# Kernel optimization log

Hardware: AMD Instinct MI355X
Metric: run time of the kernel (lower is better)

The kernel has to match this reference:

```python
import jax, jax.numpy as jnp
import numpy as np

B, T, D, H = 256, 256, 512, 8
HD = D // H  # 64


def _rope_tables(t, hd):
    pos = jnp.arange(t, dtype=jnp.float32)
    inv_freq = 1.0 / (10000.0 ** (jnp.arange(0, hd, 2, dtype=jnp.float32) / hd))
    ang = pos[:, None] * inv_freq[None, :]            # (T, hd/2)
    cos = jnp.repeat(jnp.cos(ang), 2, axis=-1)        # (T, hd) interleaved pairs
    sin = jnp.repeat(jnp.sin(ang), 2, axis=-1)
    return cos, sin


def setup_inputs() -> dict:
    key = jax.random.key(0)
    k1, k2, k3 = jax.random.split(key, 3)
    x = jax.random.normal(k1, (B, T, D), dtype=jnp.float32)
    cos, sin = _rope_tables(T, HD)
    Wqkv = jax.random.normal(k2, (3 * D, D), dtype=jnp.float32) * 0.02
    Wout = jax.random.normal(k3, (D, D), dtype=jnp.float32) * 0.02
    return {"x": x, "cos": cos, "sin": sin, "Wqkv": Wqkv, "Wout": Wout}


def _apply_rope(x, cos, sin):
    # x: (B, T, H, hd); cos/sin: (T, hd)
    x1 = x[..., 0::2]
    x2 = x[..., 1::2]
    rot = jnp.stack((-x2, x1), axis=-1).reshape(x.shape)  # interleaved rotate
    return x * cos[None, :, None, :] + rot * sin[None, :, None, :]


def reference(x, cos, sin, Wqkv, Wout):
    b, t, d = x.shape
    qkv = (x @ Wqkv.T).reshape(b, t, 3, H, HD)
    q, k, v = qkv[:, :, 0], qkv[:, :, 1], qkv[:, :, 2]   # (B, T, H, hd)
    q = _apply_rope(q, cos[:t], sin[:t])
    k = _apply_rope(k, cos[:t], sin[:t])
    q = q.transpose(0, 2, 1, 3)  # (B, H, T, hd)
    k = k.transpose(0, 2, 1, 3)
    v = v.transpose(0, 2, 1, 3)
    scale = 1.0 / jnp.sqrt(jnp.float32(HD))
    scores = jnp.einsum('bhqd,bhkd->bhqk', q, k) * scale
    causal = jnp.arange(t)[:, None] >= jnp.arange(t)[None, :]  # (T, T)
    scores = jnp.where(causal[None, None], scores, jnp.finfo(scores.dtype).min)
    att = jax.nn.softmax(scores, axis=-1)
    out = jnp.einsum('bhqk,bhkd->bhqd', att, v)          # (B, H, T, hd)
    out = out.transpose(0, 2, 1, 3).reshape(b, t, d)
    return out @ Wout.T
```

## Files before the change

kernel.cpp:

```cpp
#include <hip/hip_runtime.h>

typedef float floatx4 __attribute__((ext_vector_type(4)));
typedef short short8 __attribute__((ext_vector_type(8)));
typedef unsigned short ushort_t;

#define AS1 __attribute__((address_space(1)))
#define AS3 __attribute__((address_space(3)))

__device__ __forceinline__ void gload_lds16(const ushort_t* g, ushort_t* l) {
    __builtin_amdgcn_global_load_lds((const AS1 unsigned int*)g, (AS3 unsigned int*)l, 16, 0, 0);
}

__device__ __forceinline__ ushort_t f2bf(float f) {
    union { float f; unsigned u; } v; v.f = f;
    unsigned r = v.u + 0x7FFFu + ((v.u >> 16) & 1u);
    return (ushort_t)(r >> 16);
}

#define KDIM 512
#define LOG2E 1.44269504f

#define XB_OFF   0ull
#define ATT_OFF  0ull
#define WQKV_OFF 33554432ull
#define WOUT_OFF 34340864ull
#define QB_OFF   34603008ull
#define KB_OFF   68157440ull
#define VB_OFF   101711872ull

__global__ __launch_bounds__(256) void convert_k(
    const float* __restrict__ x, const float* __restrict__ wqkv,
    const float* __restrict__ wout, ushort_t* __restrict__ dst)
{
    size_t i = (size_t)blockIdx.x * 256 + threadIdx.x;
    size_t e = i * 4;
    const float* s; size_t o;
    if (e < 33554432ull)      { s = x;    o = e; }
    else if (e < 34340864ull) { s = wqkv; o = e - 33554432ull; }
    else                      { s = wout; o = e - 34340864ull; }
    float4 v = *(const float4*)(s + o);
    ushort4 r;
    r.x = f2bf(v.x); r.y = f2bf(v.y); r.z = f2bf(v.z); r.w = f2bf(v.w);
    *(ushort4*)(dst + e) = r;
}

template <int EPI>
__global__ __launch_bounds__(256, 3) void gemm_bt(
    const ushort_t* __restrict__ A, const ushort_t* __restrict__ Bw,
    float* __restrict__ Cf,
    ushort_t* __restrict__ qout, ushort_t* __restrict__ kout, ushort_t* __restrict__ vout,
    const float* __restrict__ cosT, const float* __restrict__ sinT)
{
    __shared__ __align__(16) ushort_t As[128 * 64];
    __shared__ __align__(16) ushort_t Bs[128 * 64];
    const int bn = blockIdx.x, bm = blockIdx.y;
    const int tid = threadIdx.x;
    const int lane = tid & 63, wave = tid >> 6;
    const int wm = wave & 1, wn = wave >> 1;
    const int quad = lane >> 4, l16 = lane & 15;

    const ushort_t* Ag = A + (size_t)bm * 128 * KDIM;
    const ushort_t* Bg = Bw + (size_t)bn * 128 * KDIM;

    floatx4 acc[4][4] = {};

    for (int k0 = 0; k0 < KDIM; k0 += 64) {
#pragma unroll
        for (int ii = 0; ii < 4; ii++) {
            int e8 = ii * 256 + tid;
            int row = e8 >> 3, col = (e8 & 7) << 3;
            gload_lds16(Ag + row * KDIM + k0 + col, &As[e8 * 8]);
            gload_lds16(Bg + row * KDIM + k0 + col, &Bs[e8 * 8]);
        }
        __syncthreads();
#pragma unroll
        for (int kk = 0; kk < 2; kk++) {
            short8 af[4], bf[4];
#pragma unroll
            for (int mi = 0; mi < 4; mi++)
                af[mi] = *(const short8*)&As[(wm * 64 + mi * 16 + l16) * 64 + kk * 32 + quad * 8];
#pragma unroll
            for (int ni = 0; ni < 4; ni++)
                bf[ni] = *(const short8*)&Bs[(wn * 64 + ni * 16 + l16) * 64 + kk * 32 + quad * 8];
#pragma unroll
            for (int mi = 0; mi < 4; mi++)
#pragma unroll
                for (int ni = 0; ni < 4; ni++)
                    acc[mi][ni] = __builtin_amdgcn_mfma_f32_16x16x32_bf16(
                        af[mi], bf[ni], acc[mi][ni], 0, 0, 0);
        }
        __syncthreads();
    }

    if constexpr (EPI == 1) {
        const int n_base = bn * 128 + wn * 64;
        const int qkv = n_base >> 9;
        ushort_t* dst = (qkv == 0) ? qout : (qkv == 1 ? kout : vout);
#pragma unroll
        for (int mi = 0; mi < 4; mi++) {
            const int m = bm * 128 + wm * 64 + mi * 16 + quad * 4;
#pragma unroll
            for (int ni = 0; ni < 4; ni++) {
                const int n = n_base + ni * 16 + l16;
                const int nw = n & 511, hd = n & 63;
#pragma unroll
                for (int r = 0; r < 4; r++) {
                    const int mm = m + r, t = mm & 255;
                    const size_t dsti = (size_t)mm * 512 + nw;
                    float val = acc[mi][ni][r];
                    if (qkv == 2) {
                        dst[dsti] = f2bf(val);
                    } else {
                        float partner = __shfl_xor(val, 1);
                        float c = cosT[t * 64 + hd], s = sinT[t * 64 + hd];
                        float o = val * c + ((hd & 1) ? partner : -partner) * s;
                        dst[dsti] = (qkv == 0) ? f2bf(o * 0.125f) : f2bf(o);
                    }
                }
            }
        }
    } else {
#pragma unroll
        for (int mi = 0; mi < 4; mi++) {
            const int m = bm * 128 + wm * 64 + mi * 16 + quad * 4;
#pragma unroll
            for (int ni = 0; ni < 4; ni++) {
                const int n = bn * 128 + wn * 64 + ni * 16 + l16;
#pragma unroll
                for (int r = 0; r < 4; r++)
                    Cf[(size_t)(m + r) * 512 + n] = acc[mi][ni][r];
            }
        }
    }
}

__global__ __launch_bounds__(256) void attn_k(
    const ushort_t* __restrict__ qb, const ushort_t* __restrict__ kb,
    const ushort_t* __restrict__ vb, ushort_t* __restrict__ attb)
{
    __shared__ __align__(16) ushort_t Ks[256 * 72];
    __shared__ __align__(16) ushort_t Vt[64 * 264];
    __shared__ __align__(16) ushort_t Ps[4 * 32 * 40];

    const int blk = blockIdx.x;
    const int qt = blk & 1, bh = blk >> 1;
    const int b = bh >> 3, h = bh & 7;
    const int tid = threadIdx.x, lane = tid & 63, w = tid >> 6;
    const int quad = lane >> 4, l16 = lane & 15;
    const int q0 = qt * 128;
    const int kend = q0 + 128;

    const ushort_t* Kg = kb + ((size_t)b * 256) * 512 + h * 64;
    const ushort_t* Vg = vb + ((size_t)b * 256) * 512 + h * 64;
    const ushort_t* Qg = qb + ((size_t)b * 256) * 512 + h * 64;

    for (int e8 = tid; e8 < kend * 8; e8 += 256) {
        int t = e8 >> 3, c = (e8 & 7) << 3;
        *(short8*)&Ks[t * 72 + c] = *(const short8*)&Kg[t * 512 + c];
        short8 vv = *(const short8*)&Vg[t * 512 + c];
#pragma unroll
        for (int j = 0; j < 8; j++) Vt[(c + j) * 264 + t] = ((const ushort_t*)&vv)[j];
    }
    __syncthreads();

    short8 qf[2][2];
#pragma unroll
    for (int mi = 0; mi < 2; mi++)
#pragma unroll
        for (int kk = 0; kk < 2; kk++)
            qf[mi][kk] = *(const short8*)&Qg[(size_t)(q0 + w * 32 + mi * 16 + l16) * 512 + kk * 32 + quad * 8];

    float lsum[2][4] = {};
    floatx4 o_[2][4] = {};

    ushort_t* Pw = &Ps[w * 32 * 40];
    const int ktdiag = qt * 4 + w;

    for (int kt = 0; kt <= ktdiag; kt++) {
        const bool diag = (kt == ktdiag);
        floatx4 s_[2][2] = {};
#pragma unroll
        for (int kk = 0; kk < 2; kk++) {
            short8 kf0 = *(const short8*)&Ks[(kt * 32 + l16) * 72 + kk * 32 + quad * 8];
            short8 kf1 = *(const short8*)&Ks[(kt * 32 + 16 + l16) * 72 + kk * 32 + quad * 8];
#pragma unroll
            for (int mi = 0; mi < 2; mi++) {
                s_[mi][0] = __builtin_amdgcn_mfma_f32_16x16x32_bf16(qf[mi][kk], kf0, s_[mi][0], 0, 0, 0);
                s_[mi][1] = __builtin_amdgcn_mfma_f32_16x16x32_bf16(qf[mi][kk], kf1, s_[mi][1], 0, 0, 0);
            }
        }
#pragma unroll
        for (int mi = 0; mi < 2; mi++) {
#pragma unroll
            for (int r = 0; r < 4; r++) {
                float p0 = exp2f(s_[mi][0][r] * LOG2E);
                float p1 = exp2f(s_[mi][1][r] * LOG2E);
                if (diag) {
                    const int rl = mi * 16 + quad * 4 + r;
                    if (l16 > rl)      p0 = 0.f;
                    if (l16 + 16 > rl) p1 = 0.f;
                }
                lsum[mi][r] += p0 + p1;
                const int rowL = mi * 16 + quad * 4 + r;
                Pw[rowL * 40 + l16] = f2bf(p0);
                Pw[rowL * 40 + 16 + l16] = f2bf(p1);
            }
        }
        __asm__ volatile("s_waitcnt lgkmcnt(0)" ::: "memory");
        short8 pf[2];
#pragma unroll
        for (int mi = 0; mi < 2; mi++)
            pf[mi] = *(const short8*)&Pw[(mi * 16 + l16) * 40 + quad * 8];
#pragma unroll
        for (int vni = 0; vni < 4; vni++) {
            short8 vf = *(const short8*)&Vt[(vni * 16 + l16) * 264 + kt * 32 + quad * 8];
#pragma unroll
            for (int mi = 0; mi < 2; mi++)
                o_[mi][vni] = __builtin_amdgcn_mfma_f32_16x16x32_bf16(pf[mi], vf, o_[mi][vni], 0, 0, 0);
        }
    }

#pragma unroll
    for (int mi = 0; mi < 2; mi++) {
#pragma unroll
        for (int r = 0; r < 4; r++) {
            float rs = lsum[mi][r];
            rs += __shfl_xor(rs, 1);
            rs += __shfl_xor(rs, 2);
            rs += __shfl_xor(rs, 4);
            rs += __shfl_xor(rs, 8);
            const float inv = 1.f / rs;
            const int t = q0 + w * 32 + mi * 16 + quad * 4 + r;
            const size_t base = ((size_t)(b * 256 + t)) * 512 + h * 64;
#pragma unroll
            for (int vni = 0; vni < 4; vni++)
                attb[base + vni * 16 + l16] = f2bf(o_[mi][vni][r] * inv);
        }
    }
}

extern "C" void kernel_launch(void* const* d_in, const int* in_sizes, int n_in,
                              void* d_out, int out_size, void* d_ws, size_t ws_size,
                              hipStream_t stream) {
    const float* x    = (const float*)d_in[0];
    const float* cosT = (const float*)d_in[1];
    const float* sinT = (const float*)d_in[2];
    const float* wqkv = (const float*)d_in[3];
    const float* wout = (const float*)d_in[4];
    float* out = (float*)d_out;
    ushort_t* ws = (ushort_t*)d_ws;

    ushort_t* xb    = ws + XB_OFF;
    ushort_t* wqkvb = ws + WQKV_OFF;
    ushort_t* woutb = ws + WOUT_OFF;
    ushort_t* qbp   = ws + QB_OFF;
    ushort_t* kbp   = ws + KB_OFF;
    ushort_t* vbp   = ws + VB_OFF;
    ushort_t* attb  = ws + ATT_OFF;

    convert_k<<<33792, 256, 0, stream>>>(x, wqkv, wout, ws);
    gemm_bt<1><<<dim3(12, 512), 256, 0, stream>>>(xb, wqkvb, nullptr, qbp, kbp, vbp, cosT, sinT);
    attn_k<<<4096, 256, 0, stream>>>(qbp, kbp, vbp, attb);
    gemm_bt<0><<<dim3(4, 512), 256, 0, stream>>>(attb, woutb, out, nullptr, nullptr, nullptr, nullptr, nullptr);
}
```

Baseline: 584.8 us.

## Enlarge GEMM tiles to 256x256 with 4-stage async LDS pipeline

Rewrites the bf16 GEMM kernel used for the QKV and output projections. Each block now computes a 256x256 tile with 512 threads, and each wave owns a 128x64 sub-tile, which increases operand reuse per LDS load. The K loop is split into 32-wide steps staged into four LDS buffers with direct global-to-LDS loads. It issues loads three steps ahead and waits on explicit vmcnt counts, with MFMA sections raised in priority, so memory latency overlaps with compute. The cost is 128KB of LDS per block, which limits occupancy to one block per CU, and fewer blocks overall, which risks tail imbalance.

```diff
diff --git a/kernel.cpp b/kernel.cpp
--- a/kernel.cpp
+++ b/kernel.cpp
@@ -44,75 +44,104 @@
     *(ushort4*)(dst + e) = r;
 }
 
+
+__device__ __forceinline__ void stage_tile(const ushort_t* __restrict__ Ag,
+    const ushort_t* __restrict__ Bg, ushort_t* As, ushort_t* Bs,
+    const int k0, const int tid)
+{
+#pragma unroll
+    for (int rnd = 0; rnd < 2; rnd++) {
+        const int e = rnd * 512 + tid;
+        const int row = e >> 2, c8 = (e & 3) << 3;
+        gload_lds16(Ag + (size_t)row * KDIM + k0 + c8, As + e * 8);
+        gload_lds16(Bg + (size_t)row * KDIM + k0 + c8, Bs + e * 8);
+    }
+}
+
+__device__ __forceinline__ void compute_tile(const ushort_t* Ab, const ushort_t* Bb,
+    floatx4 (&acc)[8][4], const int wm, const int wn, const int l16, const int quad)
+{
+    short8 af[8], bfr[4];
+#pragma unroll
+    for (int mi = 0; mi < 8; mi++)
+        af[mi] = *(const short8*)&Ab[(wm * 128 + mi * 16 + l16) * 32 + quad * 8];
+#pragma unroll
+    for (int ni = 0; ni < 4; ni++)
+        bfr[ni] = *(const short8*)&Bb[(wn * 64 + ni * 16 + l16) * 32 + quad * 8];
+    __builtin_amdgcn_s_setprio(1);
+#pragma unroll
+    for (int mi = 0; mi < 8; mi++)
+#pragma unroll
+        for (int ni = 0; ni < 4; ni++)
+            acc[mi][ni] = __builtin_amdgcn_mfma_f32_16x16x32_bf16(
+                af[mi], bfr[ni], acc[mi][ni], 0, 0, 0);
+    __builtin_amdgcn_s_setprio(0);
+}
+
+#define PHASE_END(VMSTR)                               \
+    asm volatile("s_waitcnt " VMSTR ::: "memory");     \
+    __builtin_amdgcn_s_barrier();                      \
+    __builtin_amdgcn_sched_barrier(0);
+
 template <int EPI>
-__global__ __launch_bounds__(256, 3) void gemm_bt(
+__global__ __launch_bounds__(512, 2) void gemm_bt(
     const ushort_t* __restrict__ A, const ushort_t* __restrict__ Bw,
     float* __restrict__ Cf,
     ushort_t* __restrict__ qout, ushort_t* __restrict__ kout, ushort_t* __restrict__ vout,
     const float* __restrict__ cosT, const float* __restrict__ sinT)
 {
-    __shared__ __align__(16) ushort_t As[128 * 64];
-    __shared__ __align__(16) ushort_t Bs[128 * 64];
+    __shared__ __align__(16) ushort_t As[4 * 8192];
+    __shared__ __align__(16) ushort_t Bs[4 * 8192];
     const int bn = blockIdx.x, bm = blockIdx.y;
     const int tid = threadIdx.x;
     const int lane = tid & 63, wave = tid >> 6;
-    const int wm = wave & 1, wn = wave >> 1;
+    const int wm = wave >> 2, wn = wave & 3;
     const int quad = lane >> 4, l16 = lane & 15;
 
-    const ushort_t* Ag = A + (size_t)bm * 128 * KDIM;
-    const ushort_t* Bg = Bw + (size_t)bn * 128 * KDIM;
-
-    floatx4 acc[4][4] = {};
-
-    for (int k0 = 0; k0 < KDIM; k0 += 64) {
-#pragma unroll
-        for (int ii = 0; ii < 4; ii++) {
-            int e8 = ii * 256 + tid;
-            int row = e8 >> 3, col = (e8 & 7) << 3;
-            gload_lds16(Ag + row * KDIM + k0 + col, &As[e8 * 8]);
-            gload_lds16(Bg + row * KDIM + k0 + col, &Bs[e8 * 8]);
-        }
-        __syncthreads();
-#pragma unroll
-        for (int kk = 0; kk < 2; kk++) {
-            short8 af[4], bf[4];
-#pragma unroll
-            for (int mi = 0; mi < 4; mi++)
-                af[mi] = *(const short8*)&As[(wm * 64 + mi * 16 + l16) * 64 + kk * 32 + quad * 8];
-#pragma unroll
-            for (int ni = 0; ni < 4; ni++)
-                bf[ni] = *(const short8*)&Bs[(wn * 64 + ni * 16 + l16) * 64 + kk * 32 + quad * 8];
-#pragma unroll
-            for (int mi = 0; mi < 4; mi++)
-#pragma unroll
-                for (int ni = 0; ni < 4; ni++)
-                    acc[mi][ni] = __builtin_amdgcn_mfma_f32_16x16x32_bf16(
-                        af[mi], bf[ni], acc[mi][ni], 0, 0, 0);
-        }
-        __syncthreads();
-    }
+    const ushort_t* Ag = A + (size_t)bm * 256 * KDIM;
+    const ushort_t* Bg = Bw + (size_t)bn * 256 * KDIM;
+
+    floatx4 acc[8][4] = {};
+
+    stage_tile(Ag, Bg, As, Bs, 0, tid);
+    stage_tile(Ag, Bg, As + 8192, Bs + 8192, 32, tid);
+    stage_tile(Ag, Bg, As + 16384, Bs + 16384, 64, tid);
+    PHASE_END("vmcnt(8)")
+
+#pragma unroll 1
+    for (int t = 0; t < 13; t++) {
+        const int pb = (t + 3) & 3;
+        stage_tile(Ag, Bg, As + pb * 8192, Bs + pb * 8192, (t + 3) * 32, tid);
+        compute_tile(As + (t & 3) * 8192, Bs + (t & 3) * 8192, acc, wm, wn, l16, quad);
+        PHASE_END("vmcnt(8)")
+    }
+    compute_tile(As + 1 * 8192, Bs + 1 * 8192, acc, wm, wn, l16, quad);
+    PHASE_END("vmcnt(4)")
+    compute_tile(As + 2 * 8192, Bs + 2 * 8192, acc, wm, wn, l16, quad);
+    PHASE_END("vmcnt(0)")
+    compute_tile(As + 3 * 8192, Bs + 3 * 8192, acc, wm, wn, l16, quad);
 
     if constexpr (EPI == 1) {
-        const int n_base = bn * 128 + wn * 64;
+        const int n_base = bn * 256 + wn * 64;
         const int qkv = n_base >> 9;
         ushort_t* dst = (qkv == 0) ? qout : (qkv == 1 ? kout : vout);
 #pragma unroll
-        for (int mi = 0; mi < 4; mi++) {
-            const int m = bm * 128 + wm * 64 + mi * 16 + quad * 4;
+        for (int mi = 0; mi < 8; mi++) {
+            const int m = bm * 256 + wm * 128 + mi * 16 + quad * 4;
 #pragma unroll
             for (int ni = 0; ni < 4; ni++) {
                 const int n = n_base + ni * 16 + l16;
                 const int nw = n & 511, hd = n & 63;
 #pragma unroll
                 for (int r = 0; r < 4; r++) {
-                    const int mm = m + r, t = mm & 255;
+                    const int mm = m + r, tt = mm & 255;
                     const size_t dsti = (size_t)mm * 512 + nw;
                     float val = acc[mi][ni][r];
                     if (qkv == 2) {
                         dst[dsti] = f2bf(val);
                     } else {
                         float partner = __shfl_xor(val, 1);
-                        float c = cosT[t * 64 + hd], s = sinT[t * 64 + hd];
+                        float c = cosT[tt * 64 + hd], s = sinT[tt * 64 + hd];
                         float o = val * c + ((hd & 1) ? partner : -partner) * s;
                         dst[dsti] = (qkv == 0) ? f2bf(o * 0.125f) : f2bf(o);
                     }
@@ -121,11 +150,11 @@
         }
     } else {
 #pragma unroll
-        for (int mi = 0; mi < 4; mi++) {
-            const int m = bm * 128 + wm * 64 + mi * 16 + quad * 4;
+        for (int mi = 0; mi < 8; mi++) {
+            const int m = bm * 256 + wm * 128 + mi * 16 + quad * 4;
 #pragma unroll
             for (int ni = 0; ni < 4; ni++) {
-                const int n = bn * 128 + wn * 64 + ni * 16 + l16;
+                const int n = bn * 256 + wn * 64 + ni * 16 + l16;
 #pragma unroll
                 for (int r = 0; r < 4; r++)
                     Cf[(size_t)(m + r) * 512 + n] = acc[mi][ni][r];
@@ -259,7 +288,7 @@
     ushort_t* attb  = ws + ATT_OFF;
 
     convert_k<<<33792, 256, 0, stream>>>(x, wqkv, wout, ws);
-    gemm_bt<1><<<dim3(12, 512), 256, 0, stream>>>(xb, wqkvb, nullptr, qbp, kbp, vbp, cosT, sinT);
+    gemm_bt<1><<<dim3(6, 256), 512, 0, stream>>>(xb, wqkvb, nullptr, qbp, kbp, vbp, cosT, sinT);
     attn_k<<<4096, 256, 0, stream>>>(qbp, kbp, vbp, attb);
-    gemm_bt<0><<<dim3(4, 512), 256, 0, stream>>>(attb, woutb, out, nullptr, nullptr, nullptr, nullptr, nullptr);
-}
+    gemm_bt<0><<<dim3(2, 256), 512, 0, stream>>>(attb, woutb, out, nullptr, nullptr, nullptr, nullptr, nullptr);
+}
```

Result: slower. 662.4 us (+13.3%).
